# Kernel optimization log

Measured on AMD Instinct MI355X. Metric: run time of the kernel, lower is better.

## Reference

```python
import jax, jax.numpy as jnp
import numpy as np

B, S, D, H = 4, 2048, 1024, 16
DH = D // H


def setup_inputs() -> dict:
    key = jax.random.key(0)
    k = jax.random.split(key, 5)
    scale = 1.0 / np.sqrt(D)
    return {
        "x": jax.random.normal(k[0], (B, S, D), dtype=jnp.float32),
        "WQ": jax.random.normal(k[1], (D, D), dtype=jnp.float32) * scale,
        "WK": jax.random.normal(k[2], (D, D), dtype=jnp.float32) * scale,
        "WV": jax.random.normal(k[3], (D, D), dtype=jnp.float32) * scale,
        "WO": jax.random.normal(k[4], (D, D), dtype=jnp.float32) * scale,
    }


def reference(x, WQ, WK, WV, WO):
    b, s, d = x.shape
    # nn.Linear (bias=False): y = x @ W.T, weight shape (out, in)
    q = (x @ WQ.T).reshape(b, s, H, DH).transpose(0, 2, 1, 3)  # (B,H,S,Dh)
    k = (x @ WK.T).reshape(b, s, H, DH).transpose(0, 2, 1, 3)
    v = (x @ WV.T).reshape(b, s, H, DH).transpose(0, 2, 1, 3)
    # attn_mask is None -> zeros; scale = sqrt(d_heads) (E after head split)
    scores = jnp.einsum("bhsd,bhtd->bhst", q, k) / jnp.sqrt(jnp.asarray(DH, x.dtype))
    attn = jnp.nan_to_num(jax.nn.softmax(scores, axis=-1))
    out = jnp.einsum("bhst,bhtd->bhsd", attn, v)  # (B,H,S,Dh)
    out = out.transpose(0, 2, 1, 3).reshape(b, s, d)
    return out @ WO.T
```

## Files before the change

### kernel.cpp

```cpp
#include <hip/hip_runtime.h>
#include <hip/hip_bf16.h>

#define BB 4
#define SS 2048
#define DD 1024
#define HH 16
#define DHH 64
#define MM (BB*SS)

typedef __bf16 bf16x8 __attribute__((ext_vector_type(8)));
typedef __bf16 bf16x4 __attribute__((ext_vector_type(4)));
typedef float  f32x4  __attribute__((ext_vector_type(4)));

__device__ __forceinline__ f32x4 mfma16(bf16x8 a, bf16x8 b, f32x4 c) {
    return __builtin_amdgcn_mfma_f32_16x16x32_bf16(a, b, c, 0, 0, 0);
}

__device__ __forceinline__ void async16(const void* g, void* l) {
    __builtin_amdgcn_global_load_lds(
        (const __attribute__((address_space(1))) void*)g,
        (__attribute__((address_space(3))) void*)l, 16, 0, 0);
}

__global__ __launch_bounds__(256) void cvt_f32_bf16(const float* __restrict__ s,
                                                    __bf16* __restrict__ d, int n8,
                                                    float scale) {
    int i = blockIdx.x * blockDim.x + threadIdx.x;
    if (i >= n8) return;
    float4 v0 = ((const float4*)s)[2*i];
    float4 v1 = ((const float4*)s)[2*i + 1];
    bf16x8 o = { (__bf16)(v0.x*scale), (__bf16)(v0.y*scale), (__bf16)(v0.z*scale), (__bf16)(v0.w*scale),
                 (__bf16)(v1.x*scale), (__bf16)(v1.y*scale), (__bf16)(v1.z*scale), (__bf16)(v1.w*scale) };
    ((bf16x8*)d)[i] = o;
}

template<typename OutT, bool PERM>
__global__ __launch_bounds__(256) void gemm_nt(const __bf16* __restrict__ A,
                                               const __bf16* __restrict__ Bb, size_t bStride,
                                               OutT* __restrict__ Cb, size_t cStride,
                                               int ncols) {
    constexpr int K = DD;
    __shared__ __bf16 As[128*32];
    __shared__ __bf16 Bs[128*32];
    const int t = threadIdx.x, l = t & 63, w = t >> 6;
    const int l15 = l & 15, g8 = (l >> 4) << 3;
    const int wm = w >> 1, wn = w & 1;
    const int m0 = blockIdx.y * 128, n0 = blockIdx.x * 128;
    const __bf16* Bp = Bb + (size_t)blockIdx.z * bStride;
    OutT* Cp = Cb + (size_t)blockIdx.z * cStride;

    f32x4 acc[4][4] = {};

    for (int k0 = 0; k0 < K; k0 += 32) {
        #pragma unroll
        for (int j = 0; j < 2; ++j) {
            int c0 = w*128 + j*64;
            int ca = c0 + l;
            int row = ca >> 2, kc = (ca & 3) << 3;
            async16(A  + (size_t)(m0 + row)*K + k0 + kc, &As[c0*8]);
            async16(Bp + (size_t)(n0 + row)*K + k0 + kc, &Bs[c0*8]);
        }
        __syncthreads();
        bf16x8 af[4], bfr[4];
        #pragma unroll
        for (int mi = 0; mi < 4; ++mi)
            af[mi] = *(const bf16x8*)&As[(wm*64 + mi*16 + l15)*32 + g8];
        #pragma unroll
        for (int ni = 0; ni < 4; ++ni)
            bfr[ni] = *(const bf16x8*)&Bs[(wn*64 + ni*16 + l15)*32 + g8];
        #pragma unroll
        for (int mi = 0; mi < 4; ++mi)
            #pragma unroll
            for (int ni = 0; ni < 4; ++ni)
                acc[mi][ni] = mfma16(af[mi], bfr[ni], acc[mi][ni]);
        __syncthreads();
    }
    #pragma unroll
    for (int mi = 0; mi < 4; ++mi)
        #pragma unroll
        for (int ni = 0; ni < 4; ++ni)
            #pragma unroll
            for (int r = 0; r < 4; ++r) {
                int row = m0 + wm*64 + mi*16 + ((l >> 4) << 2) + r;
                int col = n0 + wn*64 + ni*16 + l15;
                if (PERM) col = (col & ~63) | ((col & 15) << 2) | ((col >> 4) & 3);
                Cp[(size_t)row*ncols + col] = (OutT)acc[mi][ni][r];
            }
}

__global__ __launch_bounds__(256) void attn_fwd(const __bf16* __restrict__ Qm,
                                                const __bf16* __restrict__ Km,
                                                const __bf16* __restrict__ Vt,
                                                __bf16* __restrict__ AO) {
    __shared__ __bf16 Kb[2][64*64];
    __shared__ __bf16 Vb[2][64*64];
    __shared__ __bf16 Pl[4][32*64];
    const int t = threadIdx.x, l = t & 63, w = t >> 6;
    const int l15 = l & 15, g = l >> 4;
    const int bh = blockIdx.x, qt = blockIdx.y;
    const int b = bh >> 4, h = bh & 15;
    const size_t qbase = (size_t)b*SS + qt*128;

    const __bf16* Kbh = Km + (size_t)b*SS*DD + h*DHH;
    const __bf16* Vbh = Vt + (size_t)h*DHH*MM + (size_t)b*SS;

    const int ca = w*128 + l,      cb_ = w*128 + 64 + l;
    const int ra = ca >> 3,        rb = cb_ >> 3;
    const int ka = ((ca & 7) ^ (ra & 7)) << 3;
    const int kb2 = ((cb_ & 7) ^ (rb & 7)) << 3;

    bf16x8 qa[2][2];
    #pragma unroll
    for (int mi = 0; mi < 2; ++mi)
        #pragma unroll
        for (int ks = 0; ks < 2; ++ks)
            qa[mi][ks] = *(const bf16x8*)(Qm + (qbase + w*32 + mi*16 + l15)*DD
                                          + h*DHH + ks*32 + g*8);

    f32x4 Oacc[2][4] = {};
    float Lacc[8] = {0.f,0.f,0.f,0.f,0.f,0.f,0.f,0.f};

    auto stage = [&](int kv0n, int nb) {
        async16(Kbh + (size_t)(kv0n + ra)*DD + ka, &Kb[nb][(w*128)*8]);
        async16(Kbh + (size_t)(kv0n + rb)*DD + kb2, &Kb[nb][(w*128 + 64)*8]);
        async16(Vbh + (size_t)ra*MM + kv0n + ka, &Vb[nb][(w*128)*8]);
        async16(Vbh + (size_t)rb*MM + kv0n + kb2, &Vb[nb][(w*128 + 64)*8]);
    };

    stage(0, 0);
    __syncthreads();
    int cur = 0;
    for (int it = 0; it < SS/64; ++it) {
        int nx = (it + 1 < SS/64) ? (it + 1)*64 : 0;
        stage(nx, cur ^ 1);

        f32x4 sf[2][4] = {};
        #pragma unroll
        for (int ni = 0; ni < 4; ++ni) {
            int r = ni*16 + l15, sw = (r & 7) << 3;
            bf16x8 k0 = *(const bf16x8*)&Kb[cur][r*64 + ((g*8) ^ sw)];
            bf16x8 k1 = *(const bf16x8*)&Kb[cur][r*64 + ((32 + g*8) ^ sw)];
            #pragma unroll
            for (int mi = 0; mi < 2; ++mi) {
                sf[mi][ni] = mfma16(qa[mi][0], k0, sf[mi][ni]);
                sf[mi][ni] = mfma16(qa[mi][1], k1, sf[mi][ni]);
            }
        }
        #pragma unroll
        for (int mi = 0; mi < 2; ++mi)
            #pragma unroll
            for (int ni = 0; ni < 4; ++ni)
                #pragma unroll
                for (int r = 0; r < 4; ++r) {
                    float p = __builtin_amdgcn_exp2f(sf[mi][ni][r]);
                    sf[mi][ni][r] = p;
                    Lacc[mi*4 + r] += p;
                }
        #pragma unroll
        for (int mi = 0; mi < 2; ++mi)
            #pragma unroll
            for (int r = 0; r < 4; ++r) {
                int q = mi*16 + g*4 + r;
                bf16x4 pk = { (__bf16)sf[mi][0][r], (__bf16)sf[mi][1][r],
                              (__bf16)sf[mi][2][r], (__bf16)sf[mi][3][r] };
                *(bf16x4*)&Pl[w][q*64 + ((l15*4) ^ ((q & 7) << 3))] = pk;
            }
        bf16x8 pa[2][2];
        #pragma unroll
        for (int mi = 0; mi < 2; ++mi)
            #pragma unroll
            for (int ks = 0; ks < 2; ++ks)
                pa[mi][ks] = *(const bf16x8*)&Pl[w][(mi*16 + l15)*64
                                + ((ks*32 + g*8) ^ ((l15 & 7) << 3))];
        #pragma unroll
        for (int f = 0; f < 4; ++f) {
            int r = f*16 + l15, sw = (r & 7) << 3;
            bf16x8 v0 = *(const bf16x8*)&Vb[cur][r*64 + ((g*8) ^ sw)];
            bf16x8 v1 = *(const bf16x8*)&Vb[cur][r*64 + ((32 + g*8) ^ sw)];
            #pragma unroll
            for (int mi = 0; mi < 2; ++mi) {
                Oacc[mi][f] = mfma16(pa[mi][0], v0, Oacc[mi][f]);
                Oacc[mi][f] = mfma16(pa[mi][1], v1, Oacc[mi][f]);
            }
        }
        __syncthreads();
        cur ^= 1;
    }
    #pragma unroll
    for (int m = 1; m <= 8; m <<= 1)
        #pragma unroll
        for (int i = 0; i < 8; ++i)
            Lacc[i] += __shfl_xor(Lacc[i], m, 64);
    float inv[8];
    #pragma unroll
    for (int i = 0; i < 8; ++i) inv[i] = 1.0f / Lacc[i];
    #pragma unroll
    for (int mi = 0; mi < 2; ++mi)
        #pragma unroll
        for (int f = 0; f < 4; ++f)
            #pragma unroll
            for (int r = 0; r < 4; ++r) {
                size_t row = qbase + w*32 + mi*16 + g*4 + r;
                AO[row*DD + h*DHH + f*16 + l15] = (__bf16)(Oacc[mi][f][r] * inv[mi*4+r]);
            }
}

extern "C" void kernel_launch(void* const* d_in, const int* in_sizes, int n_in,
                              void* d_out, int out_size, void* d_ws, size_t ws_size,
                              hipStream_t stream) {
    const float* x  = (const float*)d_in[0];
    const float* WQ = (const float*)d_in[1];
    const float* WK = (const float*)d_in[2];
    const float* WV = (const float*)d_in[3];
    const float* WO = (const float*)d_in[4];
    float* out = (float*)d_out;

    __bf16* xbf = (__bf16*)d_ws;
    __bf16* wqb = xbf + (size_t)MM*DD;
    __bf16* wkb = wqb + (size_t)DD*DD;
    __bf16* wvb = wkb + (size_t)DD*DD;
    __bf16* wob = wvb + (size_t)DD*DD;
    __bf16* qbf = wob + (size_t)DD*DD;
    __bf16* kbf = qbf + (size_t)MM*DD;
    __bf16* vtb = kbf + (size_t)MM*DD;
    __bf16* aobf = xbf;

    const float QS = 0.125f * 1.4426950408889634f;
    cvt_f32_bf16<<<(MM*DD/8)/256, 256, 0, stream>>>(x,  xbf, MM*DD/8, 1.0f);
    cvt_f32_bf16<<<(DD*DD/8)/256, 256, 0, stream>>>(WQ, wqb, DD*DD/8, QS);
    cvt_f32_bf16<<<(DD*DD/8)/256, 256, 0, stream>>>(WK, wkb, DD*DD/8, 1.0f);
    cvt_f32_bf16<<<(DD*DD/8)/256, 256, 0, stream>>>(WV, wvb, DD*DD/8, 1.0f);
    cvt_f32_bf16<<<(DD*DD/8)/256, 256, 0, stream>>>(WO, wob, DD*DD/8, 1.0f);

    gemm_nt<__bf16, false><<<dim3(DD/128, MM/128, 2), 256, 0, stream>>>(
        xbf, wqb, (size_t)DD*DD, qbf, (size_t)MM*DD, DD);

    gemm_nt<__bf16, true><<<dim3(MM/128, DD/128, 1), 256, 0, stream>>>(
        wvb, xbf, 0, vtb, 0, MM);

    attn_fwd<<<dim3(BB*HH, SS/128), 256, 0, stream>>>(qbf, kbf, vtb, aobf);

    gemm_nt<float, false><<<dim3(DD/128, MM/128, 1), 256, 0, stream>>>(
        aobf, wob, 0, out, 0, DD);
}
```

Before: 306.9 us.

## Double attention query tile per block, add MFMA priority hints, merge weight casts

The attention kernel now gives each block 256 query rows (64 per wave), so every K/V tile loaded into LDS feeds twice as many MFMAs. The launch grid shrinks to 512 blocks, and register and LDS use per block roughly double, which may lower occupancy. s_setprio hints are placed around the MFMA bursts in both the GEMM and attention kernels. The four weight-conversion launches are merged into a single two-dimensional launch to cut launch overhead.

```diff
diff --git a/kernel.cpp b/kernel.cpp
--- a/kernel.cpp
+++ b/kernel.cpp
@@ -27,6 +27,25 @@
                                                     float scale) {
     int i = blockIdx.x * blockDim.x + threadIdx.x;
     if (i >= n8) return;
+    float4 v0 = ((const float4*)s)[2*i];
+    float4 v1 = ((const float4*)s)[2*i + 1];
+    bf16x8 o = { (__bf16)(v0.x*scale), (__bf16)(v0.y*scale), (__bf16)(v0.z*scale), (__bf16)(v0.w*scale),
+                 (__bf16)(v1.x*scale), (__bf16)(v1.y*scale), (__bf16)(v1.z*scale), (__bf16)(v1.w*scale) };
+    ((bf16x8*)d)[i] = o;
+}
+
+__global__ __launch_bounds__(256) void cvt_w4(const float* __restrict__ w0,
+                                              const float* __restrict__ w1,
+                                              const float* __restrict__ w2,
+                                              const float* __restrict__ w3,
+                                              __bf16* __restrict__ d0,
+                                              __bf16* __restrict__ d1,
+                                              __bf16* __restrict__ d2,
+                                              __bf16* __restrict__ d3) {
+    int i = blockIdx.x * blockDim.x + threadIdx.x;
+    const float* s = blockIdx.y == 0 ? w0 : blockIdx.y == 1 ? w1 : blockIdx.y == 2 ? w2 : w3;
+    __bf16* d      = blockIdx.y == 0 ? d0 : blockIdx.y == 1 ? d1 : blockIdx.y == 2 ? d2 : d3;
+    float scale = blockIdx.y == 0 ? 0.125f * 1.4426950408889634f : 1.0f;
     float4 v0 = ((const float4*)s)[2*i];
     float4 v1 = ((const float4*)s)[2*i + 1];
     bf16x8 o = { (__bf16)(v0.x*scale), (__bf16)(v0.y*scale), (__bf16)(v0.z*scale), (__bf16)(v0.w*scale),
@@ -68,11 +87,13 @@
         #pragma unroll
         for (int ni = 0; ni < 4; ++ni)
             bfr[ni] = *(const bf16x8*)&Bs[(wn*64 + ni*16 + l15)*32 + g8];
+        __builtin_amdgcn_s_setprio(1);
         #pragma unroll
         for (int mi = 0; mi < 4; ++mi)
             #pragma unroll
             for (int ni = 0; ni < 4; ++ni)
                 acc[mi][ni] = mfma16(af[mi], bfr[ni], acc[mi][ni]);
+        __builtin_amdgcn_s_setprio(0);
         __syncthreads();
     }
     #pragma unroll
@@ -94,12 +115,12 @@
                                                 __bf16* __restrict__ AO) {
     __shared__ __bf16 Kb[2][64*64];
     __shared__ __bf16 Vb[2][64*64];
-    __shared__ __bf16 Pl[4][32*64];
+    __shared__ __bf16 Pl[4][64*64];
     const int t = threadIdx.x, l = t & 63, w = t >> 6;
     const int l15 = l & 15, g = l >> 4;
     const int bh = blockIdx.x, qt = blockIdx.y;
     const int b = bh >> 4, h = bh & 15;
-    const size_t qbase = (size_t)b*SS + qt*128;
+    const size_t qbase = (size_t)b*SS + qt*256;
 
     const __bf16* Kbh = Km + (size_t)b*SS*DD + h*DHH;
     const __bf16* Vbh = Vt + (size_t)h*DHH*MM + (size_t)b*SS;
@@ -109,16 +130,18 @@
     const int ka = ((ca & 7) ^ (ra & 7)) << 3;
     const int kb2 = ((cb_ & 7) ^ (rb & 7)) << 3;
 
-    bf16x8 qa[2][2];
-    #pragma unroll
-    for (int mi = 0; mi < 2; ++mi)
+    bf16x8 qa[4][2];
+    #pragma unroll
+    for (int mi = 0; mi < 4; ++mi)
         #pragma unroll
         for (int ks = 0; ks < 2; ++ks)
-            qa[mi][ks] = *(const bf16x8*)(Qm + (qbase + w*32 + mi*16 + l15)*DD
+            qa[mi][ks] = *(const bf16x8*)(Qm + (qbase + w*64 + mi*16 + l15)*DD
                                           + h*DHH + ks*32 + g*8);
 
-    f32x4 Oacc[2][4] = {};
-    float Lacc[8] = {0.f,0.f,0.f,0.f,0.f,0.f,0.f,0.f};
+    f32x4 Oacc[4][4] = {};
+    float Lacc[16];
+    #pragma unroll
+    for (int i = 0; i < 16; ++i) Lacc[i] = 0.f;
 
     auto stage = [&](int kv0n, int nb) {
         async16(Kbh + (size_t)(kv0n + ra)*DD + ka, &Kb[nb][(w*128)*8]);
@@ -134,20 +157,22 @@
         int nx = (it + 1 < SS/64) ? (it + 1)*64 : 0;
         stage(nx, cur ^ 1);
 
-        f32x4 sf[2][4] = {};
+        f32x4 sf[4][4] = {};
         #pragma unroll
         for (int ni = 0; ni < 4; ++ni) {
             int r = ni*16 + l15, sw = (r & 7) << 3;
             bf16x8 k0 = *(const bf16x8*)&Kb[cur][r*64 + ((g*8) ^ sw)];
             bf16x8 k1 = *(const bf16x8*)&Kb[cur][r*64 + ((32 + g*8) ^ sw)];
-            #pragma unroll
-            for (int mi = 0; mi < 2; ++mi) {
+            __builtin_amdgcn_s_setprio(1);
+            #pragma unroll
+            for (int mi = 0; mi < 4; ++mi) {
                 sf[mi][ni] = mfma16(qa[mi][0], k0, sf[mi][ni]);
                 sf[mi][ni] = mfma16(qa[mi][1], k1, sf[mi][ni]);
             }
+            __builtin_amdgcn_s_setprio(0);
         }
         #pragma unroll
-        for (int mi = 0; mi < 2; ++mi)
+        for (int mi = 0; mi < 4; ++mi)
             #pragma unroll
             for (int ni = 0; ni < 4; ++ni)
                 #pragma unroll
@@ -157,7 +182,7 @@
                     Lacc[mi*4 + r] += p;
                 }
         #pragma unroll
-        for (int mi = 0; mi < 2; ++mi)
+        for (int mi = 0; mi < 4; ++mi)
             #pragma unroll
             for (int r = 0; r < 4; ++r) {
                 int q = mi*16 + g*4 + r;
@@ -165,9 +190,9 @@
                               (__bf16)sf[mi][2][r], (__bf16)sf[mi][3][r] };
                 *(bf16x4*)&Pl[w][q*64 + ((l15*4) ^ ((q & 7) << 3))] = pk;
             }
-        bf16x8 pa[2][2];
-        #pragma unroll
-        for (int mi = 0; mi < 2; ++mi)
+        bf16x8 pa[4][2];
+        #pragma unroll
+        for (int mi = 0; mi < 4; ++mi)
             #pragma unroll
             for (int ks = 0; ks < 2; ++ks)
                 pa[mi][ks] = *(const bf16x8*)&Pl[w][(mi*16 + l15)*64
@@ -177,11 +202,13 @@
             int r = f*16 + l15, sw = (r & 7) << 3;
             bf16x8 v0 = *(const bf16x8*)&Vb[cur][r*64 + ((g*8) ^ sw)];
             bf16x8 v1 = *(const bf16x8*)&Vb[cur][r*64 + ((32 + g*8) ^ sw)];
-            #pragma unroll
-            for (int mi = 0; mi < 2; ++mi) {
+            __builtin_amdgcn_s_setprio(1);
+            #pragma unroll
+            for (int mi = 0; mi < 4; ++mi) {
                 Oacc[mi][f] = mfma16(pa[mi][0], v0, Oacc[mi][f]);
                 Oacc[mi][f] = mfma16(pa[mi][1], v1, Oacc[mi][f]);
             }
+            __builtin_amdgcn_s_setprio(0);
         }
         __syncthreads();
         cur ^= 1;
@@ -189,18 +216,18 @@
     #pragma unroll
     for (int m = 1; m <= 8; m <<= 1)
         #pragma unroll
-        for (int i = 0; i < 8; ++i)
+        for (int i = 0; i < 16; ++i)
             Lacc[i] += __shfl_xor(Lacc[i], m, 64);
-    float inv[8];
-    #pragma unroll
-    for (int i = 0; i < 8; ++i) inv[i] = 1.0f / Lacc[i];
-    #pragma unroll
-    for (int mi = 0; mi < 2; ++mi)
+    float inv[16];
+    #pragma unroll
+    for (int i = 0; i < 16; ++i) inv[i] = 1.0f / Lacc[i];
+    #pragma unroll
+    for (int mi = 0; mi < 4; ++mi)
         #pragma unroll
         for (int f = 0; f < 4; ++f)
             #pragma unroll
             for (int r = 0; r < 4; ++r) {
-                size_t row = qbase + w*32 + mi*16 + g*4 + r;
+                size_t row = qbase + w*64 + mi*16 + g*4 + r;
                 AO[row*DD + h*DHH + f*16 + l15] = (__bf16)(Oacc[mi][f][r] * inv[mi*4+r]);
             }
 }
@@ -225,12 +252,9 @@
     __bf16* vtb = kbf + (size_t)MM*DD;
     __bf16* aobf = xbf;
 
-    const float QS = 0.125f * 1.4426950408889634f;
-    cvt_f32_bf16<<<(MM*DD/8)/256, 256, 0, stream>>>(x,  xbf, MM*DD/8, 1.0f);
-    cvt_f32_bf16<<<(DD*DD/8)/256, 256, 0, stream>>>(WQ, wqb, DD*DD/8, QS);
-    cvt_f32_bf16<<<(DD*DD/8)/256, 256, 0, stream>>>(WK, wkb, DD*DD/8, 1.0f);
-    cvt_f32_bf16<<<(DD*DD/8)/256, 256, 0, stream>>>(WV, wvb, DD*DD/8, 1.0f);
-    cvt_f32_bf16<<<(DD*DD/8)/256, 256, 0, stream>>>(WO, wob, DD*DD/8, 1.0f);
+    cvt_f32_bf16<<<(MM*DD/8)/256, 256, 0, stream>>>(x, xbf, MM*DD/8, 1.0f);
+    cvt_w4<<<dim3((DD*DD/8)/256, 4), 256, 0, stream>>>(WQ, WK, WV, WO,
+                                                       wqb, wkb, wvb, wob);
 
     gemm_nt<__bf16, false><<<dim3(DD/128, MM/128, 2), 256, 0, stream>>>(
         xbf, wqb, (size_t)DD*DD, qbf, (size_t)MM*DD, DD);
@@ -238,7 +262,7 @@
     gemm_nt<__bf16, true><<<dim3(MM/128, DD/128, 1), 256, 0, stream>>>(
         wvb, xbf, 0, vtb, 0, MM);
 
-    attn_fwd<<<dim3(BB*HH, SS/128), 256, 0, stream>>>(qbf, kbf, vtb, aobf);
+    attn_fwd<<<dim3(BB*HH, SS/256), 256, 0, stream>>>(qbf, kbf, vtb, aobf);
 
     gemm_nt<float, false><<<dim3(DD/128, MM/128, 1), 256, 0, stream>>>(
         aobf, wob, 0, out, 0, DD);
```

Measured after the change: 333.1 us. 1.09x slower.
